# Optimization experiments

Measured on AMD Instinct MI355X. Metric: run time of the kernel, lower is better.

Reference implementation:

```python
import jax, jax.numpy as jnp
import numpy as np
import math

MAX_L = 3
E, R, C = 100000, 8, 16  # num_edges, n_radial, n_chanel


def _l_list(max_l):
    # all monomial exponent triples (lx,ly,lz) with lx+ly+lz <= max_l,
    # in the nested-loop order used for init_kwargs l_list
    return [(lx, ly, lz)
            for lx in range(max_l + 1)
            for ly in range(max_l + 1 - lx)
            for lz in range(max_l + 1 - lx - ly)]


def _combo_indices(max_l):
    # find_combo_vectors_l1l2: for every l3 in l_list, every componentwise
    # decomposition l3 = l1 + l2, with integer binomial prefactor
    ll = _l_list(max_l)
    idx = {t: i for i, t in enumerate(ll)}
    l3s, l1s, l2s, pf = [], [], [], []
    for l3 in ll:
        for a in range(l3[0] + 1):
            for b in range(l3[1] + 1):
                for c in range(l3[2] + 1):
                    l1 = (a, b, c)
                    l2 = (l3[0] - a, l3[1] - b, l3[2] - c)
                    l3s.append(idx[l3])
                    l1s.append(idx[l1])
                    l2s.append(idx[l2])
                    pf.append(math.comb(l3[0], a) * math.comb(l3[1], b) * math.comb(l3[2], c))
    return (np.asarray(l3s, np.int32), np.asarray(l1s, np.int32),
            np.asarray(l2s, np.int32), np.asarray(pf, np.float32))


def setup_inputs() -> dict:
    key = jax.random.key(0)
    k1, k2 = jax.random.split(key)
    A = len(_l_list(MAX_L))  # n_angular = 20
    edge_attr1 = jax.random.normal(k1, (E, R, A, C), dtype=jnp.float32)
    edge_attr2 = jax.random.normal(k2, (E, R, A, C), dtype=jnp.float32)
    l3_idx, l1_idx, l2_idx, prefactor = _combo_indices(MAX_L)
    return {
        "edge_attr1": edge_attr1,
        "edge_attr2": edge_attr2,
        "l3_idx": jnp.asarray(l3_idx),
        "l1_idx": jnp.asarray(l1_idx),
        "l2_idx": jnp.asarray(l2_idx),
        "prefactor": jnp.asarray(prefactor),
    }


def reference(edge_attr1, edge_attr2, l3_idx, l1_idx, l2_idx, prefactor):
    # vectorized gather-multiply-scale over all K=84 (l1,l2,l3) combos,
    # then one scatter-add into the l3 angular slot
    terms = (prefactor[None, None, :, None]
             * edge_attr1[:, :, l1_idx, :]
             * edge_attr2[:, :, l2_idx, :])  # [E, R, K, C]
    out = jnp.zeros_like(edge_attr1).at[:, :, l3_idx, :].add(terms)
    return out
```

## Files before the change

kernel.cpp:

```cpp
#include <hip/hip_runtime.h>


#define NA 20
#define NK 84
#define TR 8
#define ROWQ 80
#define PADQ 82
#define NTH 128

typedef float f32x4 __attribute__((ext_vector_type(4)));

namespace atp {

constexpr int lidx(int x, int y, int z) {
  int i = 0;
  for (int a = 0; a < x; ++a) i += (4 - a) * (5 - a) / 2;
  for (int b = 0; b < y; ++b) i += 4 - x - b;
  return i + z;
}

constexpr int combi(int n, int k) {
  int r = 1;
  for (int i = 1; i <= k; ++i) r = r * (n - k + i) / i;
  return r;
}

struct Tab {
  int l1[NK];
  int l2[NK];
  float pf[NK];
  int cnt[NA];
  int off[NA];
};

constexpr Tab make_tab() {
  Tab t{};
  int n = 0, m = 0;
  for (int x = 0; x <= 3; ++x)
    for (int y = 0; y <= 3 - x; ++y)
      for (int z = 0; z <= 3 - x - y; ++z) {
        t.off[m] = n;
        t.cnt[m] = (x + 1) * (y + 1) * (z + 1);
        for (int a = 0; a <= x; ++a)
          for (int b = 0; b <= y; ++b)
            for (int c = 0; c <= z; ++c) {
              t.l1[n] = lidx(a, b, c);
              t.l2[n] = lidx(x - a, y - b, z - c);
              t.pf[n] = (float)(combi(x, a) * combi(y, b) * combi(z, c));
              ++n;
            }
        ++m;
      }
  return t;
}

constexpr Tab T = make_tab();

}

__global__ __launch_bounds__(NTH) void atp_kernel(
    const float* __restrict__ in1, const float* __restrict__ in2,
    float* __restrict__ out) {
  __shared__ f32x4 lds1[TR * PADQ];
  __shared__ f32x4 lds2[TR * PADQ];

  const int t = threadIdx.x;
  const long base_q = (long)blockIdx.x * (TR * ROWQ);
  const f32x4* g1 = reinterpret_cast<const f32x4*>(in1) + base_q;
  const f32x4* g2 = reinterpret_cast<const f32x4*>(in2) + base_q;

#pragma unroll
  for (int k = 0; k < 5; ++k) {
    const int q = k * NTH + t;
    const int row = q / ROWQ;
    const int qq = q - row * ROWQ;
    lds1[row * PADQ + qq] = __builtin_nontemporal_load(g1 + q);
    lds2[row * PADQ + qq] = __builtin_nontemporal_load(g2 + q);
  }
  __syncthreads();

  const int row = t >> 4;
  const int c = t & 15;
  const float* l1p = reinterpret_cast<const float*>(lds1) + row * (PADQ * 4) + c;
  const float* l2p = reinterpret_cast<const float*>(lds2) + row * (PADQ * 4) + c;
  float* op = out + base_q * 4 + row * (ROWQ * 4) + c;

  float v1[NA], v2[NA];
#pragma unroll
  for (int a = 0; a < NA; ++a) v1[a] = l1p[a * 16];
#pragma unroll
  for (int a = 0; a < NA; ++a) v2[a] = l2p[a * 16];

#pragma unroll
  for (int i3 = 0; i3 < NA; ++i3) {
    float acc = 0.f;
#pragma unroll
    for (int j = 0; j < atp::T.cnt[i3]; ++j) {
      const int k = atp::T.off[i3] + j;
      acc = fmaf(atp::T.pf[k] * v1[atp::T.l1[k]], v2[atp::T.l2[k]], acc);
    }
    op[i3 * 16] = acc;
  }
}

extern "C" void kernel_launch(void* const* d_in, const int* in_sizes, int n_in,
                              void* d_out, int out_size, void* d_ws, size_t ws_size,
                              hipStream_t stream) {
  const float* in1 = (const float*)d_in[0];
  const float* in2 = (const float*)d_in[1];
  float* out = (float*)d_out;
  const int n_tiles = out_size / (TR * NA * 16);
  atp_kernel<<<n_tiles, NTH, 0, stream>>>(in1, in2, out);
}
```

Baseline: 552.3 us.

## Pipeline tiles with async global-to-LDS loads and double buffering per block

Each block now processes 25 tiles in a loop, not one. The next tile is prefetched into a second LDS buffer with direct global_load_lds while the current tile is computed. An XOR swizzle on odd rows replaces the LDS padding to avoid bank conflicts. The aim is to hide HBM latency and cut launch/staging overhead. In exchange the grid is much smaller, so fewer waves are available to hide latency, and the block count silently assumes the tile count divides evenly by 25.

```diff
diff --git a/kernel.cpp b/kernel.cpp
--- a/kernel.cpp
+++ b/kernel.cpp
@@ -1,12 +1,15 @@
 #include <hip/hip_runtime.h>
+#include <stdint.h>
 
 
 #define NA 20
 #define NK 84
 #define TR 8
-#define ROWQ 80
-#define PADQ 82
+#define ROWF 320
+#define TILEF (TR*ROWF)
+#define TILEQ (TILEF/4)
 #define NTH 128
+#define GPB 25
 
 typedef float f32x4 __attribute__((ext_vector_type(4)));
 
@@ -26,11 +29,7 @@
 }
 
 struct Tab {
-  int l1[NK];
-  int l2[NK];
-  float pf[NK];
-  int cnt[NA];
-  int off[NA];
+  int l1[NK]; int l2[NK]; float pf[NK]; int cnt[NA]; int off[NA];
 };
 
 constexpr Tab make_tab() {
@@ -58,48 +57,71 @@
 
 }
 
+__device__ __forceinline__ void stage_tile(const f32x4* __restrict__ g1,
+                                           const f32x4* __restrict__ g2,
+                                           float* ldsbuf, int t) {
+#pragma unroll
+  for (int k = 0; k < 5; ++k) {
+    const int Q = k * NTH + t;
+    const int row = Q / 80;
+    const int Qs = Q ^ ((row & 1) << 2);
+    __builtin_amdgcn_global_load_lds(
+        (const __attribute__((address_space(1))) uint32_t*)(g1 + Qs),
+        (__attribute__((address_space(3))) uint32_t*)(ldsbuf + Q * 4), 16, 0, 0);
+    __builtin_amdgcn_global_load_lds(
+        (const __attribute__((address_space(1))) uint32_t*)(g2 + Qs),
+        (__attribute__((address_space(3))) uint32_t*)(ldsbuf + TILEF + Q * 4), 16, 0, 0);
+  }
+}
+
 __global__ __launch_bounds__(NTH) void atp_kernel(
     const float* __restrict__ in1, const float* __restrict__ in2,
     float* __restrict__ out) {
-  __shared__ f32x4 lds1[TR * PADQ];
-  __shared__ f32x4 lds2[TR * PADQ];
+  __shared__ float lds[2][2][TILEF];
 
   const int t = threadIdx.x;
-  const long base_q = (long)blockIdx.x * (TR * ROWQ);
-  const f32x4* g1 = reinterpret_cast<const f32x4*>(in1) + base_q;
-  const f32x4* g2 = reinterpret_cast<const f32x4*>(in2) + base_q;
+  const int r = t >> 4;
+  const int c = t & 15;
+  const int rx = r & 1;
+  const long tile0 = (long)blockIdx.x * GPB;
 
+  const f32x4* g1 = reinterpret_cast<const f32x4*>(in1) + tile0 * TILEQ;
+  const f32x4* g2 = reinterpret_cast<const f32x4*>(in2) + tile0 * TILEQ;
+
+  stage_tile(g1, g2, &lds[0][0][0], t);
+
+  int buf = 0;
+  for (int g = 0; g < GPB; ++g) {
+    if (g + 1 < GPB) {
+      stage_tile(g1 + (g + 1) * TILEQ, g2 + (g + 1) * TILEQ,
+                 &lds[buf ^ 1][0][0], t);
+      asm volatile("s_waitcnt vmcnt(10)" ::: "memory");
+    } else {
+      asm volatile("s_waitcnt vmcnt(0)" ::: "memory");
+    }
+    __builtin_amdgcn_s_barrier();
+
+    const float* l1p = &lds[buf][0][r * ROWF];
+    const float* l2p = &lds[buf][1][r * ROWF];
+    float v1[NA], v2[NA];
 #pragma unroll
-  for (int k = 0; k < 5; ++k) {
-    const int q = k * NTH + t;
-    const int row = q / ROWQ;
-    const int qq = q - row * ROWQ;
-    lds1[row * PADQ + qq] = __builtin_nontemporal_load(g1 + q);
-    lds2[row * PADQ + qq] = __builtin_nontemporal_load(g2 + q);
-  }
-  __syncthreads();
+    for (int a = 0; a < NA; ++a) v1[a] = l1p[((a ^ rx) << 4) + c];
+#pragma unroll
+    for (int a = 0; a < NA; ++a) v2[a] = l2p[((a ^ rx) << 4) + c];
 
-  const int row = t >> 4;
-  const int c = t & 15;
-  const float* l1p = reinterpret_cast<const float*>(lds1) + row * (PADQ * 4) + c;
-  const float* l2p = reinterpret_cast<const float*>(lds2) + row * (PADQ * 4) + c;
-  float* op = out + base_q * 4 + row * (ROWQ * 4) + c;
-
-  float v1[NA], v2[NA];
+    float* op = out + (tile0 + g) * TILEF + r * ROWF + c;
 #pragma unroll
-  for (int a = 0; a < NA; ++a) v1[a] = l1p[a * 16];
+    for (int i3 = 0; i3 < NA; ++i3) {
+      float acc = 0.f;
 #pragma unroll
-  for (int a = 0; a < NA; ++a) v2[a] = l2p[a * 16];
-
-#pragma unroll
-  for (int i3 = 0; i3 < NA; ++i3) {
-    float acc = 0.f;
-#pragma unroll
-    for (int j = 0; j < atp::T.cnt[i3]; ++j) {
-      const int k = atp::T.off[i3] + j;
-      acc = fmaf(atp::T.pf[k] * v1[atp::T.l1[k]], v2[atp::T.l2[k]], acc);
+      for (int j = 0; j < atp::T.cnt[i3]; ++j) {
+        const int k = atp::T.off[i3] + j;
+        acc = fmaf(atp::T.pf[k] * v1[atp::T.l1[k]], v2[atp::T.l2[k]], acc);
+      }
+      op[i3 * 16] = acc;
     }
-    op[i3 * 16] = acc;
+    __builtin_amdgcn_s_barrier();
+    buf ^= 1;
   }
 }
 
@@ -109,6 +131,7 @@
   const float* in1 = (const float*)d_in[0];
   const float* in2 = (const float*)d_in[1];
   float* out = (float*)d_out;
-  const int n_tiles = out_size / (TR * NA * 16);
-  atp_kernel<<<n_tiles, NTH, 0, stream>>>(in1, in2, out);
+  const int n_tiles = out_size / TILEF;
+  const int blocks = n_tiles / GPB;
+  atp_kernel<<<blocks, NTH, 0, stream>>>(in1, in2, out);
 }
```

After: 609.4 us. 10.3% more time.
